# Kernel tuning notes

Measured on AMD Instinct MI355X. Metric: run time of the kernel, lower is better.

Reference implementation:

```python
import jax, jax.numpy as jnp
import numpy as np


def setup_inputs() -> dict:
    key = jax.random.key(0)
    ks = jax.random.split(key, 8)
    B, Te, De, Dd, H = 64, 1024, 1024, 1024, 1024
    return {
        "encoder_outputs": jax.random.normal(ks[0], (B, Te, De), jnp.float32),
        "decoder_outputs": jax.random.normal(ks[1], (B, 1, Dd), jnp.float32),
        "Wa_w": jax.random.normal(ks[2], (H, Dd), jnp.float32) * 0.02,
        "Wa_b": jax.random.normal(ks[3], (H,), jnp.float32) * 0.02,
        "Ua_w": jax.random.normal(ks[4], (H, De), jnp.float32) * 0.02,
        "Ua_b": jax.random.normal(ks[5], (H,), jnp.float32) * 0.02,
        "Va_w": jax.random.normal(ks[6], (1, H), jnp.float32) * 0.02,
        "Va_b": jax.random.normal(ks[7], (1,), jnp.float32) * 0.02,
    }


def reference(encoder_outputs, decoder_outputs, Wa_w, Wa_b, Ua_w, Ua_b, Va_w, Va_b):
    # Wa: [B,1,H], Ua: [B,Te,H]  (torch Linear: x @ W.T + b)
    Wa = jnp.einsum('bqd,hd->bqh', decoder_outputs, Wa_w) + Wa_b
    Ua = jnp.einsum('bed,hd->beh', encoder_outputs, Ua_w) + Ua_b
    # broadcast add -> tanh -> scalar score per encoder position: [B,Te,1]
    scores = jnp.einsum('beh,oh->beo', jnp.tanh(Wa + Ua), Va_w) + Va_b
    scores = jnp.transpose(scores, (0, 2, 1))          # [B,1,Te]
    weights = jax.nn.softmax(scores, axis=-1)          # softmax over Te
    context = jnp.einsum('bqe,bed->bqd', weights, encoder_outputs)  # [B,1,De]
    return context
```

## Files before the change

### kernel.cpp

```cpp
#include <hip/hip_runtime.h>
#include <hip/hip_bf16.h>

#define B_  64
#define TE  1024
#define K_  1024
#define HH  1024
#define MM  (B_ * TE)

typedef __bf16 bf16x8 __attribute__((ext_vector_type(8)));
typedef __bf16 bf16x4 __attribute__((ext_vector_type(4)));
typedef float  f32x4  __attribute__((ext_vector_type(4)));

__device__ __forceinline__ float fast_tanh(float x) {
    float ax = __builtin_fabsf(x);
    float t  = __expf(-2.0f * ax);
    float r  = (1.0f - t) * __builtin_amdgcn_rcpf(1.0f + t);
    return __builtin_copysignf(r, x);
}

__global__ void cvt_kernel(const float* __restrict__ in, __bf16* __restrict__ out, long n4) {
    long i = (long)blockIdx.x * blockDim.x + threadIdx.x;
    long stride = (long)gridDim.x * blockDim.x;
    const float4* in4 = (const float4*)in;
    bf16x4* out4 = (bf16x4*)out;
    for (long j = i; j < n4; j += stride) {
        float4 v = in4[j];
        bf16x4 o;
        o[0] = (__bf16)v.x; o[1] = (__bf16)v.y; o[2] = (__bf16)v.z; o[3] = (__bf16)v.w;
        out4[j] = o;
    }
}

__global__ void wa_kernel(const float* __restrict__ dec, const float* __restrict__ Wa_w,
                          const float* __restrict__ Wa_b, float* __restrict__ WaOut) {
    int b = blockIdx.x, ht = blockIdx.y;
    int wave = threadIdx.x >> 6, lane = threadIdx.x & 63;
    const float* db = dec + b * 1024;
    for (int i = 0; i < 16; i++) {
        int h = ht * 64 + wave * 16 + i;
        const float* wr = Wa_w + (long)h * 1024;
        float a = 0.0f;
        #pragma unroll
        for (int k = 0; k < 16; k++)
            a += db[lane + 64 * k] * wr[lane + 64 * k];
        #pragma unroll
        for (int off = 32; off > 0; off >>= 1)
            a += __shfl_xor(a, off, 64);
        if (lane == 0) WaOut[b * 1024 + h] = a + Wa_b[h];
    }
}

#define MT 128
#define NP 256
#define KT 64

__global__ __launch_bounds__(256, 2) void score_gemm(
    const __bf16* __restrict__ A,
    const __bf16* __restrict__ Bm,
    const float* __restrict__ Wa,
    const float* __restrict__ Ua_b,
    const float* __restrict__ Va_w,
    float* __restrict__ scores)
{
    __shared__ __bf16 sA[MT * KT];
    __shared__ __bf16 sB[NP * KT];
    __shared__ float sVa[NP];
    __shared__ float sWU[NP];

    const int tid  = threadIdx.x;
    const int wave = tid >> 6;
    const int lane = tid & 63;
    const int quad = lane >> 4;
    const int l16  = lane & 15;
    const int wm   = wave >> 1;
    const int wn   = wave & 1;

    const int bid = blockIdx.x;
    const int grp = bid >> 5;
    const int r5  = bid & 31;
    const int y   = r5 >> 3;
    const int x   = grp * 8 + (r5 & 7);

    const int rowBase = x * MT;
    const int colBase = y * NP;
    const int b       = rowBase >> 10;

    if (tid < NP) {
        int h = colBase + tid;
        sVa[tid] = Va_w[h];
        sWU[tid] = Wa[b * 1024 + h] + Ua_b[h];
    }

    f32x4 acc[4][8] = {};

    const long aBase = (long)rowBase * K_;
    const long bBase = (long)colBase * K_;

    for (int k0 = 0; k0 < K_; k0 += KT) {
        __syncthreads();
        #pragma unroll
        for (int i = 0; i < 4; i++) {
            int c = i * 256 + tid;
            int r = c >> 3, slot = c & 7;
            int seg = slot ^ (r & 7);
            __builtin_amdgcn_global_load_lds(
                (const __attribute__((address_space(1))) unsigned int*)(A + aBase + (long)r * K_ + k0 + seg * 8),
                (__attribute__((address_space(3))) unsigned int*)(sA + c * 8), 16, 0, 0);
        }
        #pragma unroll
        for (int i = 0; i < 8; i++) {
            int c = i * 256 + tid;
            int r = c >> 3, slot = c & 7;
            int seg = slot ^ (r & 7);
            __builtin_amdgcn_global_load_lds(
                (const __attribute__((address_space(1))) unsigned int*)(Bm + bBase + (long)r * K_ + k0 + seg * 8),
                (__attribute__((address_space(3))) unsigned int*)(sB + c * 8), 16, 0, 0);
        }
        __syncthreads();

        #pragma unroll
        for (int ks = 0; ks < 2; ks++) {
            bf16x8 bfr[8];
            #pragma unroll
            for (int t = 0; t < 8; t++) {
                int r = wn * 128 + t * 16 + l16;
                int slot = (ks * 4 + quad) ^ (r & 7);
                bfr[t] = *(const bf16x8*)(sB + r * KT + slot * 8);
            }
            #pragma unroll
            for (int s = 0; s < 4; s++) {
                int r = wm * 64 + s * 16 + l16;
                int slot = (ks * 4 + quad) ^ (r & 7);
                bf16x8 af = *(const bf16x8*)(sA + r * KT + slot * 8);
                #pragma unroll
                for (int t = 0; t < 8; t++)
                    acc[s][t] = __builtin_amdgcn_mfma_f32_16x16x32_bf16(af, bfr[t], acc[s][t], 0, 0, 0);
            }
        }
    }

    float rs[4][4] = {};
    #pragma unroll
    for (int s = 0; s < 4; s++)
        #pragma unroll
        for (int t = 0; t < 8; t++) {
            int hl = wn * 128 + t * 16 + l16;
            float va = sVa[hl], wu = sWU[hl];
            #pragma unroll
            for (int r = 0; r < 4; r++)
                rs[s][r] += va * fast_tanh(acc[s][t][r] + wu);
        }

    #pragma unroll
    for (int s = 0; s < 4; s++)
        #pragma unroll
        for (int r = 0; r < 4; r++) {
            float v = rs[s][r];
            v += __shfl_xor(v, 1, 64);
            v += __shfl_xor(v, 2, 64);
            v += __shfl_xor(v, 4, 64);
            v += __shfl_xor(v, 8, 64);
            if (l16 == 0)
                atomicAdd(&scores[rowBase + wm * 64 + s * 16 + quad * 4 + r], v);
        }
}

__global__ void softmax_kernel(float* __restrict__ s) {
    __shared__ float red[256];
    int b = blockIdx.x, tid = threadIdx.x;
    float4* row = (float4*)(s + b * 1024);
    float4 v = row[tid];
    float m = fmaxf(fmaxf(v.x, v.y), fmaxf(v.z, v.w));
    red[tid] = m; __syncthreads();
    for (int off = 128; off > 0; off >>= 1) {
        if (tid < off) red[tid] = fmaxf(red[tid], red[tid + off]);
        __syncthreads();
    }
    m = red[0]; __syncthreads();
    v.x = expf(v.x - m); v.y = expf(v.y - m); v.z = expf(v.z - m); v.w = expf(v.w - m);
    red[tid] = v.x + v.y + v.z + v.w; __syncthreads();
    for (int off = 128; off > 0; off >>= 1) {
        if (tid < off) red[tid] += red[tid + off];
        __syncthreads();
    }
    float inv = 1.0f / red[0];
    v.x *= inv; v.y *= inv; v.z *= inv; v.w *= inv;
    row[tid] = v;
}

__global__ void context_kernel(const __bf16* __restrict__ enc, const float* __restrict__ w,
                               float* __restrict__ out) {
    int b = blockIdx.x, ec = blockIdx.y, tid = threadIdx.x;
    const bf16x4* enc4 = (const bf16x4*)(enc + ((long)b * 1024 + ec * 64) * 1024);
    const float* wrow = w + b * 1024 + ec * 64;
    float ax = 0, ay = 0, az = 0, aw = 0;
    for (int e = 0; e < 64; e++) {
        float we = wrow[e];
        bf16x4 v = enc4[e * 256 + tid];
        ax += we * (float)v[0]; ay += we * (float)v[1];
        az += we * (float)v[2]; aw += we * (float)v[3];
    }
    float* o = out + b * 1024 + tid * 4;
    atomicAdd(o + 0, ax); atomicAdd(o + 1, ay);
    atomicAdd(o + 2, az); atomicAdd(o + 3, aw);
}

extern "C" void kernel_launch(void* const* d_in, const int* in_sizes, int n_in,
                              void* d_out, int out_size, void* d_ws, size_t ws_size,
                              hipStream_t stream) {
    (void)in_sizes; (void)n_in; (void)ws_size;
    const float* enc   = (const float*)d_in[0];
    const float* dec   = (const float*)d_in[1];
    const float* Wa_w  = (const float*)d_in[2];
    const float* Wa_b  = (const float*)d_in[3];
    const float* Ua_w  = (const float*)d_in[4];
    const float* Ua_b  = (const float*)d_in[5];
    const float* Va_w  = (const float*)d_in[6];
    float* out = (float*)d_out;

    char* w = (char*)d_ws;
    __bf16* encB = (__bf16*)w;  w += (size_t)MM * 1024 * 2;
    __bf16* uawB = (__bf16*)w;  w += (size_t)HH * 1024 * 2;
    float* WaBuf = (float*)w;   w += (size_t)B_ * HH * 4;
    float* scores = (float*)w;  w += (size_t)MM * 4;

    hipMemsetAsync(scores, 0, (size_t)MM * 4, stream);
    hipMemsetAsync(out, 0, (size_t)out_size * 4, stream);
    cvt_kernel<<<dim3(4096), 256, 0, stream>>>(enc, encB, (long)MM * 1024 / 4);
    cvt_kernel<<<dim3(256), 256, 0, stream>>>(Ua_w, uawB, (long)HH * 1024 / 4);
    wa_kernel<<<dim3(B_, 16), 256, 0, stream>>>(dec, Wa_w, Wa_b, WaBuf);
    score_gemm<<<dim3((MM / MT) * (HH / NP)), 256, 0, stream>>>(encB, uawB, WaBuf, Ua_b, Va_w, scores);
    softmax_kernel<<<dim3(B_), 256, 0, stream>>>(scores);
    context_kernel<<<dim3(B_, 16), 256, 0, stream>>>(encB, scores, out);
}
```

Before: 587.9 us.

## Fuse encoder fp32-to-bf16 conversion into score GEMM A-tile loading

Drops the separate conversion pass over the encoder outputs. The score GEMM now reads the fp32 encoder tile directly through registers, converts it to bf16 and stores it to LDS, and the y==0 column blocks also write the bf16 copy that the context kernel still reads. A register prefetch of the next K tile overlaps the fp32 loads with the MFMA work. In exchange, every column block reads twice as many bytes for A, the async LDS DMA load is replaced by register staging that raises register pressure, and the y==0 blocks carry extra global writes.

New measurement: 528.2 us. 1.11x faster.

```diff
diff --git a/kernel.cpp b/kernel.cpp
--- a/kernel.cpp
+++ b/kernel.cpp
@@ -55,7 +55,8 @@
 #define KT 64
 
 __global__ __launch_bounds__(256, 2) void score_gemm(
-    const __bf16* __restrict__ A,
+    const float* __restrict__ Af,
+    __bf16* __restrict__ encB,
     const __bf16* __restrict__ Bm,
     const float* __restrict__ Wa,
     const float* __restrict__ Ua_b,
@@ -84,6 +85,7 @@
     const int rowBase = x * MT;
     const int colBase = y * NP;
     const int b       = rowBase >> 10;
+    const bool wb     = (y == 0);
 
     if (tid < NP) {
         int h = colBase + tid;
@@ -91,21 +93,38 @@
         sWU[tid] = Wa[b * 1024 + h] + Ua_b[h];
     }
 
+    int rr[4], sg[4];
+    #pragma unroll
+    for (int i = 0; i < 4; i++) {
+        int c = i * 256 + tid;
+        rr[i] = c >> 3;
+        sg[i] = (c & 7) ^ (rr[i] & 7);
+    }
+
     f32x4 acc[4][8] = {};
 
     const long aBase = (long)rowBase * K_;
     const long bBase = (long)colBase * K_;
 
+    float4 pre[4][2];
+    #pragma unroll
+    for (int i = 0; i < 4; i++) {
+        const float4* p = (const float4*)(Af + aBase + (long)rr[i] * K_ + sg[i] * 8);
+        pre[i][0] = p[0]; pre[i][1] = p[1];
+    }
+
     for (int k0 = 0; k0 < K_; k0 += KT) {
         __syncthreads();
         #pragma unroll
         for (int i = 0; i < 4; i++) {
-            int c = i * 256 + tid;
-            int r = c >> 3, slot = c & 7;
-            int seg = slot ^ (r & 7);
-            __builtin_amdgcn_global_load_lds(
-                (const __attribute__((address_space(1))) unsigned int*)(A + aBase + (long)r * K_ + k0 + seg * 8),
-                (__attribute__((address_space(3))) unsigned int*)(sA + c * 8), 16, 0, 0);
+            bf16x8 v;
+            v[0] = (__bf16)pre[i][0].x; v[1] = (__bf16)pre[i][0].y;
+            v[2] = (__bf16)pre[i][0].z; v[3] = (__bf16)pre[i][0].w;
+            v[4] = (__bf16)pre[i][1].x; v[5] = (__bf16)pre[i][1].y;
+            v[6] = (__bf16)pre[i][1].z; v[7] = (__bf16)pre[i][1].w;
+            *(bf16x8*)(sA + (i * 256 + tid) * 8) = v;
+            if (wb)
+                *(bf16x8*)(encB + aBase + (long)rr[i] * K_ + k0 + sg[i] * 8) = v;
         }
         #pragma unroll
         for (int i = 0; i < 8; i++) {
@@ -117,6 +136,14 @@
                 (__attribute__((address_space(3))) unsigned int*)(sB + c * 8), 16, 0, 0);
         }
         __syncthreads();
+
+        if (k0 + KT < K_) {
+            #pragma unroll
+            for (int i = 0; i < 4; i++) {
+                const float4* p = (const float4*)(Af + aBase + (long)rr[i] * K_ + (k0 + KT) + sg[i] * 8);
+                pre[i][0] = p[0]; pre[i][1] = p[1];
+            }
+        }
 
         #pragma unroll
         for (int ks = 0; ks < 2; ks++) {
@@ -226,10 +253,9 @@
 
     hipMemsetAsync(scores, 0, (size_t)MM * 4, stream);
     hipMemsetAsync(out, 0, (size_t)out_size * 4, stream);
-    cvt_kernel<<<dim3(4096), 256, 0, stream>>>(enc, encB, (long)MM * 1024 / 4);
     cvt_kernel<<<dim3(256), 256, 0, stream>>>(Ua_w, uawB, (long)HH * 1024 / 4);
     wa_kernel<<<dim3(B_, 16), 256, 0, stream>>>(dec, Wa_w, Wa_b, WaBuf);
-    score_gemm<<<dim3((MM / MT) * (HH / NP)), 256, 0, stream>>>(encB, uawB, WaBuf, Ua_b, Va_w, scores);
+    score_gemm<<<dim3((MM / MT) * (HH / NP)), 256, 0, stream>>>(enc, encB, uawB, WaBuf, Ua_b, Va_w, scores);
     softmax_kernel<<<dim3(B_), 256, 0, stream>>>(scores);
     context_kernel<<<dim3(B_, 16), 256, 0, stream>>>(encB, scores, out);
 }
```

## Fuse encoder bf16 conversion into score GEMM and stream pre-tiled weights from global

Applied to the files above, without the earlier changes.

The separate fp32-to-bf16 pass over the whole encoder tensor is removed. The score GEMM now loads fp32 encoder tiles, converts them in registers, double-buffers them in LDS with register prefetch, and has the y==0 column blocks write the bf16 copy that the context kernel later reads. Ua_w is repacked into an MFMA-fragment-ordered layout, so each wave loads its B fragments straight from global/L2 into registers and the B tile no longer goes through LDS. The aim is to save a full read and write pass over the encoder and to cut LDS traffic. In exchange, A is now read as fp32 by four column blocks, which doubles A bytes per block, and the K tile is halved, which adds more barriers.

Result: no change. 583.9 us (-0.7%).

```diff
diff --git a/kernel.cpp b/kernel.cpp
--- a/kernel.cpp
+++ b/kernel.cpp
@@ -18,17 +18,16 @@
     return __builtin_copysignf(r, x);
 }
 
-__global__ void cvt_kernel(const float* __restrict__ in, __bf16* __restrict__ out, long n4) {
-    long i = (long)blockIdx.x * blockDim.x + threadIdx.x;
-    long stride = (long)gridDim.x * blockDim.x;
-    const float4* in4 = (const float4*)in;
-    bf16x4* out4 = (bf16x4*)out;
-    for (long j = i; j < n4; j += stride) {
-        float4 v = in4[j];
-        bf16x4 o;
-        o[0] = (__bf16)v.x; o[1] = (__bf16)v.y; o[2] = (__bf16)v.z; o[3] = (__bf16)v.w;
-        out4[j] = o;
-    }
+__global__ void bt_kernel(const float* __restrict__ Uw, __bf16* __restrict__ Bt) {
+    int i = blockIdx.x * 256 + threadIdx.x;
+    int kc = i & 127, h = i >> 7;
+    const float4* src = (const float4*)(Uw + (long)h * 1024 + kc * 8);
+    float4 a = src[0], b = src[1];
+    bf16x8 v;
+    v[0] = (__bf16)a.x; v[1] = (__bf16)a.y; v[2] = (__bf16)a.z; v[3] = (__bf16)a.w;
+    v[4] = (__bf16)b.x; v[5] = (__bf16)b.y; v[6] = (__bf16)b.z; v[7] = (__bf16)b.w;
+    long dst = ((long)((h >> 4) * 32 + (kc >> 2)) * 512) + (kc & 3) * 128 + (h & 15) * 8;
+    *(bf16x8*)(Bt + dst) = v;
 }
 
 __global__ void wa_kernel(const float* __restrict__ dec, const float* __restrict__ Wa_w,
@@ -52,18 +51,19 @@
 
 #define MT 128
 #define NP 256
-#define KT 64
+#define KT 32
+#define NIT (K_ / KT)
 
 __global__ __launch_bounds__(256, 2) void score_gemm(
-    const __bf16* __restrict__ A,
-    const __bf16* __restrict__ Bm,
+    const float* __restrict__ Af,
+    __bf16* __restrict__ encB,
+    const __bf16* __restrict__ Bt,
     const float* __restrict__ Wa,
     const float* __restrict__ Ua_b,
     const float* __restrict__ Va_w,
     float* __restrict__ scores)
 {
-    __shared__ __bf16 sA[MT * KT];
-    __shared__ __bf16 sB[NP * KT];
+    __shared__ __bf16 sA[2][MT * KT];
     __shared__ float sVa[NP];
     __shared__ float sWU[NP];
 
@@ -84,59 +84,85 @@
     const int rowBase = x * MT;
     const int colBase = y * NP;
     const int b       = rowBase >> 10;
-
-    if (tid < NP) {
-        int h = colBase + tid;
-        sVa[tid] = Va_w[h];
-        sWU[tid] = Wa[b * 1024 + h] + Ua_b[h];
-    }
+    const bool wb     = (y == 0);
+
+    sVa[tid] = Va_w[colBase + tid];
+    sWU[tid] = Wa[b * 1024 + colBase + tid] + Ua_b[colBase + tid];
+
+    int rA[2], sgA[2], cc[2];
+    #pragma unroll
+    for (int i = 0; i < 2; i++) {
+        cc[i]  = i * 256 + tid;
+        rA[i]  = cc[i] >> 2;
+        sgA[i] = (cc[i] & 3) ^ ((rA[i] >> 1) & 3);
+    }
+
+    const long aBase = (long)rowBase * K_;
+    const int  tb0   = (colBase >> 4) + wn * 8;
 
     f32x4 acc[4][8] = {};
 
-    const long aBase = (long)rowBase * K_;
-    const long bBase = (long)colBase * K_;
-
-    for (int k0 = 0; k0 < K_; k0 += KT) {
+    {
+        #pragma unroll
+        for (int i = 0; i < 2; i++) {
+            const float4* p = (const float4*)(Af + aBase + (long)rA[i] * K_ + sgA[i] * 8);
+            float4 a = p[0], bq = p[1];
+            bf16x8 v;
+            v[0] = (__bf16)a.x;  v[1] = (__bf16)a.y;  v[2] = (__bf16)a.z;  v[3] = (__bf16)a.w;
+            v[4] = (__bf16)bq.x; v[5] = (__bf16)bq.y; v[6] = (__bf16)bq.z; v[7] = (__bf16)bq.w;
+            *(bf16x8*)(&sA[0][0] + cc[i] * 8) = v;
+            if (wb) *(bf16x8*)(encB + aBase + (long)rA[i] * K_ + sgA[i] * 8) = v;
+        }
+    }
+    __syncthreads();
+
+    bf16x8 bcur[8];
+    #pragma unroll
+    for (int t = 0; t < 8; t++)
+        bcur[t] = *(const bf16x8*)(Bt + ((long)(tb0 + t) * 32 + 0) * 512 + lane * 8);
+
+    #pragma unroll 2
+    for (int it = 0; it < NIT; it++) {
+        const int cur = it & 1;
+
+        float4 pn[2][2];
+        bf16x8 bnext[8];
+        if (it < NIT - 1) {
+            #pragma unroll
+            for (int i = 0; i < 2; i++) {
+                const float4* p = (const float4*)(Af + aBase + (long)rA[i] * K_ + (it + 1) * KT + sgA[i] * 8);
+                pn[i][0] = p[0]; pn[i][1] = p[1];
+            }
+            #pragma unroll
+            for (int t = 0; t < 8; t++)
+                bnext[t] = *(const bf16x8*)(Bt + ((long)(tb0 + t) * 32 + (it + 1)) * 512 + lane * 8);
+        }
+
+        #pragma unroll
+        for (int s = 0; s < 4; s++) {
+            int r  = wm * 64 + s * 16 + l16;
+            int ps = quad ^ ((r >> 1) & 3);
+            bf16x8 af = *(const bf16x8*)(&sA[cur][0] + r * KT + ps * 8);
+            #pragma unroll
+            for (int t = 0; t < 8; t++)
+                acc[s][t] = __builtin_amdgcn_mfma_f32_16x16x32_bf16(af, bcur[t], acc[s][t], 0, 0, 0);
+        }
+
+        if (it < NIT - 1) {
+            #pragma unroll
+            for (int i = 0; i < 2; i++) {
+                bf16x8 v;
+                v[0] = (__bf16)pn[i][0].x; v[1] = (__bf16)pn[i][0].y;
+                v[2] = (__bf16)pn[i][0].z; v[3] = (__bf16)pn[i][0].w;
+                v[4] = (__bf16)pn[i][1].x; v[5] = (__bf16)pn[i][1].y;
+                v[6] = (__bf16)pn[i][1].z; v[7] = (__bf16)pn[i][1].w;
+                *(bf16x8*)(&sA[1 - cur][0] + cc[i] * 8) = v;
+                if (wb) *(bf16x8*)(encB + aBase + (long)rA[i] * K_ + (it + 1) * KT + sgA[i] * 8) = v;
+            }
+            #pragma unroll
+            for (int t = 0; t < 8; t++) bcur[t] = bnext[t];
+        }
         __syncthreads();
-        #pragma unroll
-        for (int i = 0; i < 4; i++) {
-            int c = i * 256 + tid;
-            int r = c >> 3, slot = c & 7;
-            int seg = slot ^ (r & 7);
-            __builtin_amdgcn_global_load_lds(
-                (const __attribute__((address_space(1))) unsigned int*)(A + aBase + (long)r * K_ + k0 + seg * 8),
-                (__attribute__((address_space(3))) unsigned int*)(sA + c * 8), 16, 0, 0);
-        }
-        #pragma unroll
-        for (int i = 0; i < 8; i++) {
-            int c = i * 256 + tid;
-            int r = c >> 3, slot = c & 7;
-            int seg = slot ^ (r & 7);
-            __builtin_amdgcn_global_load_lds(
-                (const __attribute__((address_space(1))) unsigned int*)(Bm + bBase + (long)r * K_ + k0 + seg * 8),
-                (__attribute__((address_space(3))) unsigned int*)(sB + c * 8), 16, 0, 0);
-        }
-        __syncthreads();
-
-        #pragma unroll
-        for (int ks = 0; ks < 2; ks++) {
-            bf16x8 bfr[8];
-            #pragma unroll
-            for (int t = 0; t < 8; t++) {
-                int r = wn * 128 + t * 16 + l16;
-                int slot = (ks * 4 + quad) ^ (r & 7);
-                bfr[t] = *(const bf16x8*)(sB + r * KT + slot * 8);
-            }
-            #pragma unroll
-            for (int s = 0; s < 4; s++) {
-                int r = wm * 64 + s * 16 + l16;
-                int slot = (ks * 4 + quad) ^ (r & 7);
-                bf16x8 af = *(const bf16x8*)(sA + r * KT + slot * 8);
-                #pragma unroll
-                for (int t = 0; t < 8; t++)
-                    acc[s][t] = __builtin_amdgcn_mfma_f32_16x16x32_bf16(af, bfr[t], acc[s][t], 0, 0, 0);
-            }
-        }
     }
 
     float rs[4][4] = {};
@@ -220,16 +246,15 @@
 
     char* w = (char*)d_ws;
     __bf16* encB = (__bf16*)w;  w += (size_t)MM * 1024 * 2;
-    __bf16* uawB = (__bf16*)w;  w += (size_t)HH * 1024 * 2;
+    __bf16* BtB  = (__bf16*)w;  w += (size_t)HH * 1024 * 2;
     float* WaBuf = (float*)w;   w += (size_t)B_ * HH * 4;
     float* scores = (float*)w;  w += (size_t)MM * 4;
 
     hipMemsetAsync(scores, 0, (size_t)MM * 4, stream);
     hipMemsetAsync(out, 0, (size_t)out_size * 4, stream);
-    cvt_kernel<<<dim3(4096), 256, 0, stream>>>(enc, encB, (long)MM * 1024 / 4);
-    cvt_kernel<<<dim3(256), 256, 0, stream>>>(Ua_w, uawB, (long)HH * 1024 / 4);
+    bt_kernel<<<dim3(512), 256, 0, stream>>>(Ua_w, BtB);
     wa_kernel<<<dim3(B_, 16), 256, 0, stream>>>(dec, Wa_w, Wa_b, WaBuf);
-    score_gemm<<<dim3((MM / MT) * (HH / NP)), 256, 0, stream>>>(encB, uawB, WaBuf, Ua_b, Va_w, scores);
+    score_gemm<<<dim3((MM / MT) * (HH / NP)), 256, 0, stream>>>(enc, encB, BtB, WaBuf, Ua_b, Va_w, scores);
     softmax_kernel<<<dim3(B_), 256, 0, stream>>>(scores);
     context_kernel<<<dim3(B_, 16), 256, 0, stream>>>(encB, scores, out);
 }
```
